# Performance work log

Hardware: AMD Instinct MI355X
Metric: run time of the kernel (lower is better)

## Reference

```python
import jax, jax.numpy as jnp
import numpy as np
from jax import lax

B, N, NIN, NOUT, K = 8, 4096, 64, 128, 32
RATIO, R = 0.25, 0.15
M = int(N * RATIO)
DIM = NIN + 4       # x_j concat 4 point-pair features


def setup_inputs() -> dict:
    key = jax.random.key(0)
    ks = jax.random.split(key, 10)
    x = jax.random.normal(ks[0], (B, N, NIN), jnp.float32)
    pos = jax.random.uniform(ks[1], (B, N, 3), jnp.float32)
    nrm = jax.random.normal(ks[2], (B, N, 3), jnp.float32)
    norm = nrm / jnp.linalg.norm(nrm, axis=-1, keepdims=True)
    batch = jnp.broadcast_to(jnp.arange(B, dtype=jnp.int32)[:, None], (B, N))
    s = 0.05
    W1 = jax.random.normal(ks[3], (DIM, DIM), jnp.float32) * s
    b1 = jnp.zeros((DIM,), jnp.float32)
    W2 = jax.random.normal(ks[4], (DIM, DIM), jnp.float32) * s
    b2 = jnp.zeros((DIM,), jnp.float32)
    W3 = jax.random.normal(ks[5], (DIM, NOUT), jnp.float32) * s
    b3 = jnp.zeros((NOUT,), jnp.float32)
    return dict(x=x, pos=pos, norm=norm, batch=batch,
                W1=W1, b1=b1, W2=W2, b2=b2, W3=W3, b3=b3)


def fps(pos):
    """Farthest point sampling, deterministic start at index 0. pos: [N,3] -> [M] int32."""
    n = pos.shape[0]
    def step(carry, _):
        dists, last = carry
        d = jnp.sum((pos - pos[last]) ** 2, axis=-1)
        dists = jnp.minimum(dists, d)
        nxt = jnp.argmax(dists).astype(jnp.int32)
        return (dists, nxt), last
    init = (jnp.full((n,), jnp.inf, pos.dtype), jnp.int32(0))
    (_, _), idx = lax.scan(step, init, None, length=M)
    return idx


def _angle(v1, v2):
    c = jnp.cross(v1, v2)
    return jnp.arctan2(jnp.linalg.norm(c, axis=-1), jnp.sum(v1 * v2, axis=-1))


def reference(x, pos, norm, batch, W1, b1, W2, b2, W3, b3):
    # batch is implicit in the leading B dim (equal-size clouds); arg kept for parity.
    idx = jax.vmap(fps)(pos)                                   # [B,M]
    pos_s = jnp.take_along_axis(pos, idx[..., None], axis=1)   # [B,M,3]
    norm_s = jnp.take_along_axis(norm, idx[..., None], axis=1) # [B,M,3]

    # radius neighbor search: K nearest within R per sampled center
    d2 = jnp.sum((pos_s[:, :, None, :] - pos[:, None, :, :]) ** 2, axis=-1)  # [B,M,N]
    masked = jnp.where(d2 <= R * R, d2, jnp.inf)
    negv, nbr = lax.top_k(-masked, K)                          # [B,M,K]
    valid = jnp.isfinite(negv)                                 # self always valid (d2=0)

    gather = jax.vmap(lambda a, i: a[i])                       # per-batch fancy gather
    x_j = gather(x, nbr)        # [B,M,K,NIN]
    pos_j = gather(pos, nbr)    # [B,M,K,3]
    norm_j = gather(norm, nbr)  # [B,M,K,3]

    d = pos_j - pos_s[:, :, None, :]                           # pos_j - pos_i
    n_i = jnp.broadcast_to(norm_s[:, :, None, :], norm_j.shape)
    ppf = jnp.stack([
        jnp.linalg.norm(d, axis=-1),
        _angle(n_i, d),
        _angle(norm_j, d),
        _angle(n_i, norm_j),
    ], axis=-1)                                                # [B,M,K,4]

    msg = jnp.concatenate([x_j, ppf], axis=-1)                 # [B,M,K,DIM]
    h = jax.nn.relu(msg @ W1 + b1)
    h = jax.nn.relu(h @ W2 + b2)
    h = jnp.where(valid[..., None], h, -jnp.inf)
    agg = jnp.max(h, axis=2)                                   # max aggregation [B,M,DIM]
    out = jax.nn.relu(agg @ W3 + b3)                           # global_nn [B,M,NOUT]
    return out, pos_s, idx
```

## Files before the change

kernel.cpp:

```cpp
#include <hip/hip_runtime.h>
#include <hip/hip_bf16.h>
#include <math.h>

#define BB 8
#define NN 4096
#define NIN 64
#define NOUTF 128
#define KNB 32
#define MM 1024
#define DIM 68
#define CAP 320

typedef float f32x2 __attribute__((ext_vector_type(2)));

__device__ __forceinline__ f32x2 pk_add(f32x2 a, f32x2 b)
{
    f32x2 d;
    asm("v_pk_add_f32 %0, %1, %2" : "=v"(d) : "v"(a), "v"(b));
    return d;
}
__device__ __forceinline__ f32x2 pk_mul(f32x2 a, f32x2 b)
{
    f32x2 d;
    asm("v_pk_mul_f32 %0, %1, %2" : "=v"(d) : "v"(a), "v"(b));
    return d;
}

__device__ __forceinline__ f32x2 pkmax(f32x2 a, f32x2 b)
{
    f32x2 r; r.x = fmaxf(a.x, b.x); r.y = fmaxf(a.y, b.y); return r;
}

template <int CTRL>
__device__ __forceinline__ float dppmax(float v)
{
    int m = __builtin_amdgcn_update_dpp(__float_as_int(v), __float_as_int(v),
                                        CTRL, 0xF, 0xF, false);
    return fmaxf(v, __int_as_float(m));
}

__global__ __launch_bounds__(256) void fps_kernel(
    const float* __restrict__ pos,
    int* __restrict__ idx_ws,
    float* __restrict__ out_pos_s, float* __restrict__ out_idx)
{
#pragma clang fp contract(off)
    __shared__ float4 posL[NN];
    __shared__ f32x2  slot[2][4];

    const int b    = blockIdx.x;
    const int tid  = threadIdx.x;
    const int wv   = tid >> 6;
    const int lane = tid & 63;
    const float* pb = pos + (size_t)b * NN * 3;

    f32x2 X[8], Y[8], Z[8], D[8];
#pragma unroll
    for (int j = 0; j < 8; ++j) {
        int pA = tid * 16 + 2 * j;
        X[j].x = pb[pA * 3 + 0]; X[j].y = pb[pA * 3 + 3];
        Y[j].x = pb[pA * 3 + 1]; Y[j].y = pb[pA * 3 + 4];
        Z[j].x = pb[pA * 3 + 2]; Z[j].y = pb[pA * 3 + 5];
        D[j].x = INFINITY;       D[j].y = INFINITY;
    }
#pragma unroll
    for (int j = 0; j < 16; ++j) {
        int p2 = tid + 256 * j;
        posL[p2] = make_float4(pb[p2 * 3 + 0], pb[p2 * 3 + 1],
                               pb[p2 * 3 + 2], 0.0f);
    }
    __syncthreads();

    int   last = 0;
    float lx = pb[0], ly = pb[1], lz = pb[2];

#pragma unroll 2
    for (int t = 0; t < MM; ++t) {
        if (tid == 0) {
            int base = b * MM + t;
            idx_ws[base]  = last;
            out_idx[base] = (float)last;
            out_pos_s[base * 3 + 0] = lx;
            out_pos_s[base * 3 + 1] = ly;
            out_pos_s[base * 3 + 2] = lz;
        }

        float nx = -lx, ny = -ly, nz = -lz;
        f32x2 nx2; nx2.x = nx; nx2.y = nx;
        f32x2 ny2; ny2.x = ny; ny2.y = ny;
        f32x2 nz2; nz2.x = nz; nz2.y = nz;

#pragma unroll
        for (int j = 0; j < 8; ++j) {
            f32x2 dx = pk_add(X[j], nx2);
            f32x2 dy = pk_add(Y[j], ny2);
            f32x2 dz = pk_add(Z[j], nz2);
            f32x2 xx = pk_mul(dx, dx);
            f32x2 yy = pk_mul(dy, dy);
            f32x2 zz = pk_mul(dz, dz);
            f32x2 s  = pk_add(pk_add(xx, yy), zz);
            D[j].x = fminf(D[j].x, s.x);
            D[j].y = fminf(D[j].y, s.y);
        }
        f32x2 m0 = pkmax(pkmax(D[0], D[1]), pkmax(D[2], D[3]));
        f32x2 m1 = pkmax(pkmax(D[4], D[5]), pkmax(D[6], D[7]));
        f32x2 mm = pkmax(m0, m1);
        float bv = fmaxf(mm.x, mm.y);

        int k0 = (D[0].x == bv) ? 0  : ((D[0].y == bv) ? 1  : 16);
        int k1 = (D[1].x == bv) ? 2  : ((D[1].y == bv) ? 3  : 16);
        int k2 = (D[2].x == bv) ? 4  : ((D[2].y == bv) ? 5  : 16);
        int k3 = (D[3].x == bv) ? 6  : ((D[3].y == bv) ? 7  : 16);
        int k4 = (D[4].x == bv) ? 8  : ((D[4].y == bv) ? 9  : 16);
        int k5 = (D[5].x == bv) ? 10 : ((D[5].y == bv) ? 11 : 16);
        int k6 = (D[6].x == bv) ? 12 : ((D[6].y == bv) ? 13 : 16);
        int k7 = (D[7].x == bv) ? 14 : ((D[7].y == bv) ? 15 : 16);
        k0 = min(k0, k4); k1 = min(k1, k5); k2 = min(k2, k6); k3 = min(k3, k7);
        k0 = min(k0, k2); k1 = min(k1, k3);
        int kmin = min(k0, k1);
        int p_cand = tid * 16 + kmin;

        float r = bv;
        r = dppmax<0x111>(r);
        r = dppmax<0x112>(r);
        r = dppmax<0x114>(r);
        r = dppmax<0x118>(r);
        r = dppmax<0x142>(r);
        r = dppmax<0x143>(r);
        float wmax = __int_as_float(__builtin_amdgcn_readlane(__float_as_int(r), 63));

        unsigned long long msk = __ballot(bv == wmax);
        int wl = __ffsll((long long)msk) - 1;
        int pwin_wave = __builtin_amdgcn_readlane(p_cand, wl);

        const int p_ = t & 1;
        if (lane == 0) {
            f32x2 sv; sv.x = wmax; sv.y = __int_as_float(pwin_wave);
            slot[p_][wv] = sv;
        }
        __syncthreads();

        f32x2 s0 = slot[p_][0], s1 = slot[p_][1];
        f32x2 s2 = slot[p_][2], s3 = slot[p_][3];
        float cv = s0.x; int ci = __float_as_int(s0.y);
        {
            int i1 = __float_as_int(s1.y);
            bool bt = (s1.x > cv) || (s1.x == cv && i1 < ci);
            cv = bt ? s1.x : cv; ci = bt ? i1 : ci;
        }
        {
            int i2 = __float_as_int(s2.y);
            bool bt = (s2.x > cv) || (s2.x == cv && i2 < ci);
            cv = bt ? s2.x : cv; ci = bt ? i2 : ci;
        }
        {
            int i3 = __float_as_int(s3.y);
            bool bt = (s3.x > cv) || (s3.x == cv && i3 < ci);
            cv = bt ? s3.x : cv; ci = bt ? i3 : ci;
        }

        float4 cw = posL[ci];
        last = ci; lx = cw.x; ly = cw.y; lz = cw.z;
    }
}

__global__ __launch_bounds__(256) void radius_kernel(
    const float* __restrict__ pos,
    const float* __restrict__ pos_s,
    int* __restrict__ nbr_ws, int* __restrict__ nvalid_ws)
{
    __shared__ float d2L[4][CAP];
    __shared__ int   idL[4][CAP];
    __shared__ int   cntL[4];

    const int wv = threadIdx.x >> 6, lane = threadIdx.x & 63;
    const int c = blockIdx.x * 4 + wv;
    const int b = c >> 10;
    const float RSQ = 0.0225f;

    if (lane == 0) cntL[wv] = 0;

    float cx = pos_s[c * 3 + 0];
    float cy = pos_s[c * 3 + 1];
    float cz = pos_s[c * 3 + 2];
    const float* pb = pos + (size_t)b * NN * 3;

    for (int it = 0; it < NN / 64; ++it) {
        int p = it * 64 + lane;
        float dx = __fsub_rn(cx, pb[p * 3 + 0]);
        float dy = __fsub_rn(cy, pb[p * 3 + 1]);
        float dz = __fsub_rn(cz, pb[p * 3 + 2]);
        float d2 = __fadd_rn(__fadd_rn(__fmul_rn(dx, dx), __fmul_rn(dy, dy)),
                             __fmul_rn(dz, dz));
        if (d2 <= RSQ) {
            int slot = atomicAdd(&cntL[wv], 1);
            if (slot < CAP) { d2L[wv][slot] = d2; idL[wv][slot] = p; }
        }
    }
    int n = cntL[wv];
    if (n > CAP) n = CAP;

    if (n <= KNB) {
        if (lane == 0) nvalid_ws[c] = n;
        if (lane < n) nbr_ws[c * KNB + lane] = idL[wv][lane];
    } else {
        if (lane == 0) nvalid_ws[c] = KNB;
        for (int a = lane; a < n; a += 64) {
            float da = d2L[wv][a]; int ia = idL[wv][a];
            int r = 0;
            for (int jj = 0; jj < n; ++jj) {
                float dj = d2L[wv][jj]; int ij = idL[wv][jj];
                r += (dj < da || (dj == da && ij < ia)) ? 1 : 0;
            }
            if (r < KNB) nbr_ws[c * KNB + r] = ia;
        }
    }
}

__device__ __forceinline__ float angle3(float ax, float ay, float az,
                                        float bx, float by, float bz)
{
    float cx = ay * bz - az * by;
    float cy = az * bx - ax * bz;
    float cz = ax * by - ay * bx;
    float cn = sqrtf(cx * cx + cy * cy + cz * cz);
    float dt = ax * bx + ay * by + az * bz;
    return atan2f(cn, dt);
}

__device__ __forceinline__ void layer_pass(const float* __restrict__ inL,
                                           const float* __restrict__ Ws,
                                           const float* __restrict__ bs,
                                           float* __restrict__ outL, int t)
{
    const int e = t & 63, wvi = t >> 6;
    for (int jg = wvi; jg < 17; jg += 4) {
        float ax = bs[jg * 4 + 0];
        float ay = bs[jg * 4 + 1];
        float az = bs[jg * 4 + 2];
        float aw = bs[jg * 4 + 3];
#pragma unroll 4
        for (int i = 0; i < DIM; ++i) {
            float m = inL[e * 69 + i];
            const float4 w = *reinterpret_cast<const float4*>(Ws + i * DIM + jg * 4);
            ax = fmaf(m, w.x, ax);
            ay = fmaf(m, w.y, ay);
            az = fmaf(m, w.z, az);
            aw = fmaf(m, w.w, aw);
        }
        outL[e * 69 + jg * 4 + 0] = fmaxf(ax, 0.0f);
        outL[e * 69 + jg * 4 + 1] = fmaxf(ay, 0.0f);
        outL[e * 69 + jg * 4 + 2] = fmaxf(az, 0.0f);
        outL[e * 69 + jg * 4 + 3] = fmaxf(aw, 0.0f);
    }
}

__global__ __launch_bounds__(256) void mlp_kernel(
    const float* __restrict__ x, const float* __restrict__ pos,
    const float* __restrict__ norm,
    const float* __restrict__ W1, const float* __restrict__ b1,
    const float* __restrict__ W2, const float* __restrict__ b2,
    const float* __restrict__ W3, const float* __restrict__ b3,
    const int* __restrict__ idx_ws, const float* __restrict__ pos_s,
    const int* __restrict__ nbr_ws, const int* __restrict__ nvalid_ws,
    float* __restrict__ out)
{
    __shared__ alignas(16) float W1s[DIM * DIM];
    __shared__ alignas(16) float W2s[DIM * DIM];
    __shared__ float b1s[DIM], b2s[DIM];
    __shared__ float msgL[64 * 69];
    __shared__ float h1L[64 * 69];
    __shared__ float aggL[2 * DIM];
    __shared__ int   nvL[2], jLs[64];

    const int t = threadIdx.x;
    const int cg0 = blockIdx.x * 2;

    for (int u = t; u < DIM * DIM; u += 256) { W1s[u] = W1[u]; W2s[u] = W2[u]; }
    if (t < DIM) { b1s[t] = b1[t]; b2s[t] = b2[t]; }
    if (t < 2) nvL[t] = min(nvalid_ws[cg0 + t], KNB);
    __syncthreads();

    const int e = t & 63, fc = t >> 6;
    const int lc = e >> 5, slot = e & 31;
    const int c = cg0 + lc;
    const int b = c >> 10;

    if (fc == 0) {
        int nv = nvL[lc];
        jLs[e] = (slot < nv) ? nbr_ws[c * KNB + slot] : 0;
    }
    __syncthreads();

    const int j = jLs[e];
    {
        const float* xj = x + ((size_t)b * NN + j) * NIN + fc * 16;
#pragma unroll
        for (int r = 0; r < 4; ++r) {
            float4 v = *reinterpret_cast<const float4*>(xj + r * 4);
            msgL[e * 69 + fc * 16 + r * 4 + 0] = v.x;
            msgL[e * 69 + fc * 16 + r * 4 + 1] = v.y;
            msgL[e * 69 + fc * 16 + r * 4 + 2] = v.z;
            msgL[e * 69 + fc * 16 + r * 4 + 3] = v.w;
        }
    }
    if (fc == 0) {
        float pix = pos_s[c * 3 + 0];
        float piy = pos_s[c * 3 + 1];
        float piz = pos_s[c * 3 + 2];
        int ic = idx_ws[c];
        const float* pj_ = pos  + ((size_t)b * NN + j) * 3;
        const float* nj_ = norm + ((size_t)b * NN + j) * 3;
        const float* ni_ = norm + ((size_t)b * NN + ic) * 3;
        float dx = pj_[0] - pix, dy = pj_[1] - piy, dz = pj_[2] - piz;
        float nix = ni_[0], niy = ni_[1], niz = ni_[2];
        float njx = nj_[0], njy = nj_[1], njz = nj_[2];
        msgL[e * 69 + 64] = sqrtf(dx * dx + dy * dy + dz * dz);
        msgL[e * 69 + 65] = angle3(nix, niy, niz, dx, dy, dz);
        msgL[e * 69 + 66] = angle3(njx, njy, njz, dx, dy, dz);
        msgL[e * 69 + 67] = angle3(nix, niy, niz, njx, njy, njz);
    }
    __syncthreads();

    layer_pass(msgL, W1s, b1s, h1L, t);
    __syncthreads();
    layer_pass(h1L, W2s, b2s, msgL, t);
    __syncthreads();

    if (t < 2 * DIM) {
        int cc = t / DIM, jf = t % DIM;
        int nv = nvL[cc];
        float v = -INFINITY;
        for (int s = 0; s < nv; ++s)
            v = fmaxf(v, msgL[(cc * 32 + s) * 69 + jf]);
        aggL[cc * DIM + jf] = v;
    }
    __syncthreads();

    {
        int cc = t >> 7, o = t & 127;
        int cgl = cg0 + cc;
        float acc = b3[o];
#pragma unroll 4
        for (int i = 0; i < DIM; ++i)
            acc = fmaf(aggL[cc * DIM + i], W3[i * NOUTF + o], acc);
        out[(size_t)cgl * NOUTF + o] = fmaxf(acc, 0.0f);
    }
}

extern "C" void kernel_launch(void* const* d_in, const int* in_sizes, int n_in,
                              void* d_out, int out_size, void* d_ws, size_t ws_size,
                              hipStream_t stream)
{
    const float* x    = (const float*)d_in[0];
    const float* pos  = (const float*)d_in[1];
    const float* norm = (const float*)d_in[2];
    const float* W1 = (const float*)d_in[4];
    const float* b1 = (const float*)d_in[5];
    const float* W2 = (const float*)d_in[6];
    const float* b2 = (const float*)d_in[7];
    const float* W3 = (const float*)d_in[8];
    const float* b3 = (const float*)d_in[9];

    float* out       = (float*)d_out;
    float* out_pos_s = out + (size_t)BB * MM * NOUTF;
    float* out_idx   = out_pos_s + (size_t)BB * MM * 3;

    char* ws = (char*)d_ws;
    int*   idx_ws    = (int*)ws;
    int*   nbr_ws    = (int*)(ws + 131072);
    int*   nvalid_ws = (int*)(ws + 131072 + (size_t)BB * MM * KNB * 4);

    fps_kernel<<<dim3(BB), dim3(256), 0, stream>>>(pos, idx_ws,
                                                   out_pos_s, out_idx);
    radius_kernel<<<dim3((BB * MM) / 4), dim3(256), 0, stream>>>(pos, out_pos_s,
                                                                 nbr_ws, nvalid_ws);
    mlp_kernel<<<dim3((BB * MM) / 2), dim3(256), 0, stream>>>(
        x, pos, norm, W1, b1, W2, b2, W3, b3,
        idx_ws, out_pos_s, nbr_ws, nvalid_ws, out);
}
```

Before: 1.013 ms.

## Carry winner coordinates in FPS reduction, buffer outputs, and register-block MLP layers

The FPS kernel no longer stages all positions in LDS. Each lane now picks its candidate's coordinates out of registers with a select tree and sends them through the per-wave slot, which removes the dependent LDS lookup after every iteration's barrier. Per-iteration global writes by thread 0 are replaced by LDS buffering, with one coalesced flush after the loop. The distance math is also fused into a single inline-asm block. Separately, the MLP layer pass now keeps four or five float4 accumulators per thread in a single loop over inputs, so each input value is read once instead of once per output group, at the cost of higher register pressure and a divergent fifth group in wave 0.

```diff
diff --git a/kernel.cpp b/kernel.cpp
--- a/kernel.cpp
+++ b/kernel.cpp
@@ -13,17 +13,21 @@
 
 typedef float f32x2 __attribute__((ext_vector_type(2)));
 
-__device__ __forceinline__ f32x2 pk_add(f32x2 a, f32x2 b)
-{
-    f32x2 d;
-    asm("v_pk_add_f32 %0, %1, %2" : "=v"(d) : "v"(a), "v"(b));
-    return d;
-}
-__device__ __forceinline__ f32x2 pk_mul(f32x2 a, f32x2 b)
-{
-    f32x2 d;
-    asm("v_pk_mul_f32 %0, %1, %2" : "=v"(d) : "v"(a), "v"(b));
-    return d;
+__device__ __forceinline__ f32x2 dist2pk(f32x2 X, f32x2 Y, f32x2 Z,
+                                         f32x2 nx, f32x2 ny, f32x2 nz)
+{
+    f32x2 dx, dy, dz;
+    asm("v_pk_add_f32 %0, %3, %6\n\t"
+        "v_pk_add_f32 %1, %4, %7\n\t"
+        "v_pk_add_f32 %2, %5, %8\n\t"
+        "v_pk_mul_f32 %0, %0, %0\n\t"
+        "v_pk_mul_f32 %1, %1, %1\n\t"
+        "v_pk_mul_f32 %2, %2, %2\n\t"
+        "v_pk_add_f32 %0, %0, %1\n\t"
+        "v_pk_add_f32 %0, %0, %2"
+        : "=&v"(dx), "=&v"(dy), "=&v"(dz)
+        : "v"(X), "v"(Y), "v"(Z), "v"(nx), "v"(ny), "v"(nz));
+    return dx;
 }
 
 __device__ __forceinline__ f32x2 pkmax(f32x2 a, f32x2 b)
@@ -45,8 +49,10 @@
     float* __restrict__ out_pos_s, float* __restrict__ out_idx)
 {
 #pragma clang fp contract(off)
-    __shared__ float4 posL[NN];
-    __shared__ f32x2  slot[2][4];
+    __shared__ float4 slotP[2][4];
+    __shared__ int    slotI[2][4];
+    __shared__ float4 emitP[MM];
+    __shared__ int    emitI[MM];
 
     const int b    = blockIdx.x;
     const int tid  = threadIdx.x;
@@ -63,13 +69,6 @@
         Z[j].x = pb[pA * 3 + 2]; Z[j].y = pb[pA * 3 + 5];
         D[j].x = INFINITY;       D[j].y = INFINITY;
     }
-#pragma unroll
-    for (int j = 0; j < 16; ++j) {
-        int p2 = tid + 256 * j;
-        posL[p2] = make_float4(pb[p2 * 3 + 0], pb[p2 * 3 + 1],
-                               pb[p2 * 3 + 2], 0.0f);
-    }
-    __syncthreads();
 
     int   last = 0;
     float lx = pb[0], ly = pb[1], lz = pb[2];
@@ -77,12 +76,8 @@
 #pragma unroll 2
     for (int t = 0; t < MM; ++t) {
         if (tid == 0) {
-            int base = b * MM + t;
-            idx_ws[base]  = last;
-            out_idx[base] = (float)last;
-            out_pos_s[base * 3 + 0] = lx;
-            out_pos_s[base * 3 + 1] = ly;
-            out_pos_s[base * 3 + 2] = lz;
+            emitP[t] = make_float4(lx, ly, lz, 0.0f);
+            emitI[t] = last;
         }
 
         float nx = -lx, ny = -ly, nz = -lz;
@@ -92,13 +87,7 @@
 
 #pragma unroll
         for (int j = 0; j < 8; ++j) {
-            f32x2 dx = pk_add(X[j], nx2);
-            f32x2 dy = pk_add(Y[j], ny2);
-            f32x2 dz = pk_add(Z[j], nz2);
-            f32x2 xx = pk_mul(dx, dx);
-            f32x2 yy = pk_mul(dy, dy);
-            f32x2 zz = pk_mul(dz, dz);
-            f32x2 s  = pk_add(pk_add(xx, yy), zz);
+            f32x2 s = dist2pk(X[j], Y[j], Z[j], nx2, ny2, nz2);
             D[j].x = fminf(D[j].x, s.x);
             D[j].y = fminf(D[j].y, s.y);
         }
@@ -120,6 +109,34 @@
         int kmin = min(k0, k1);
         int p_cand = tid * 16 + kmin;
 
+        int jj = kmin >> 1;
+        f32x2 xa = (jj & 1) ? X[1] : X[0];
+        f32x2 xb = (jj & 1) ? X[3] : X[2];
+        f32x2 xc = (jj & 1) ? X[5] : X[4];
+        f32x2 xd = (jj & 1) ? X[7] : X[6];
+        f32x2 xe = (jj & 2) ? xb : xa;
+        f32x2 xf = (jj & 2) ? xd : xc;
+        f32x2 xg = (jj & 4) ? xf : xe;
+        float bx = (kmin & 1) ? xg.y : xg.x;
+
+        f32x2 ya = (jj & 1) ? Y[1] : Y[0];
+        f32x2 yb = (jj & 1) ? Y[3] : Y[2];
+        f32x2 yc = (jj & 1) ? Y[5] : Y[4];
+        f32x2 yd = (jj & 1) ? Y[7] : Y[6];
+        f32x2 ye = (jj & 2) ? yb : ya;
+        f32x2 yf = (jj & 2) ? yd : yc;
+        f32x2 yg = (jj & 4) ? yf : ye;
+        float by = (kmin & 1) ? yg.y : yg.x;
+
+        f32x2 za = (jj & 1) ? Z[1] : Z[0];
+        f32x2 zb = (jj & 1) ? Z[3] : Z[2];
+        f32x2 zc = (jj & 1) ? Z[5] : Z[4];
+        f32x2 zd = (jj & 1) ? Z[7] : Z[6];
+        f32x2 ze = (jj & 2) ? zb : za;
+        f32x2 zf = (jj & 2) ? zd : zc;
+        f32x2 zg = (jj & 4) ? zf : ze;
+        float bz = (kmin & 1) ? zg.y : zg.x;
+
         float r = bv;
         r = dppmax<0x111>(r);
         r = dppmax<0x112>(r);
@@ -131,36 +148,49 @@
 
         unsigned long long msk = __ballot(bv == wmax);
         int wl = __ffsll((long long)msk) - 1;
-        int pwin_wave = __builtin_amdgcn_readlane(p_cand, wl);
 
         const int p_ = t & 1;
-        if (lane == 0) {
-            f32x2 sv; sv.x = wmax; sv.y = __int_as_float(pwin_wave);
-            slot[p_][wv] = sv;
+        if (lane == wl) {
+            slotP[p_][wv] = make_float4(bx, by, bz, bv);
+            slotI[p_][wv] = p_cand;
         }
         __syncthreads();
 
-        f32x2 s0 = slot[p_][0], s1 = slot[p_][1];
-        f32x2 s2 = slot[p_][2], s3 = slot[p_][3];
-        float cv = s0.x; int ci = __float_as_int(s0.y);
+        float4 e0 = slotP[p_][0], e1 = slotP[p_][1];
+        float4 e2 = slotP[p_][2], e3 = slotP[p_][3];
+        int    i0 = slotI[p_][0], i1 = slotI[p_][1];
+        int    i2 = slotI[p_][2], i3 = slotI[p_][3];
+
+        float cv = e0.w; int ci = i0;
+        float cx = e0.x, cy = e0.y, cz = e0.z;
         {
-            int i1 = __float_as_int(s1.y);
-            bool bt = (s1.x > cv) || (s1.x == cv && i1 < ci);
-            cv = bt ? s1.x : cv; ci = bt ? i1 : ci;
+            bool bt = (e1.w > cv) || (e1.w == cv && i1 < ci);
+            cv = bt ? e1.w : cv; ci = bt ? i1 : ci;
+            cx = bt ? e1.x : cx; cy = bt ? e1.y : cy; cz = bt ? e1.z : cz;
         }
         {
-            int i2 = __float_as_int(s2.y);
-            bool bt = (s2.x > cv) || (s2.x == cv && i2 < ci);
-            cv = bt ? s2.x : cv; ci = bt ? i2 : ci;
+            bool bt = (e2.w > cv) || (e2.w == cv && i2 < ci);
+            cv = bt ? e2.w : cv; ci = bt ? i2 : ci;
+            cx = bt ? e2.x : cx; cy = bt ? e2.y : cy; cz = bt ? e2.z : cz;
         }
         {
-            int i3 = __float_as_int(s3.y);
-            bool bt = (s3.x > cv) || (s3.x == cv && i3 < ci);
-            cv = bt ? s3.x : cv; ci = bt ? i3 : ci;
-        }
-
-        float4 cw = posL[ci];
-        last = ci; lx = cw.x; ly = cw.y; lz = cw.z;
+            bool bt = (e3.w > cv) || (e3.w == cv && i3 < ci);
+            cv = bt ? e3.w : cv; ci = bt ? i3 : ci;
+            cx = bt ? e3.x : cx; cy = bt ? e3.y : cy; cz = bt ? e3.z : cz;
+        }
+        last = ci; lx = cx; ly = cy; lz = cz;
+    }
+
+    __syncthreads();
+    for (int u = tid; u < MM; u += 256) {
+        float4 rec = emitP[u];
+        int    id  = emitI[u];
+        int base = b * MM + u;
+        idx_ws[base]  = id;
+        out_idx[base] = (float)id;
+        out_pos_s[base * 3 + 0] = rec.x;
+        out_pos_s[base * 3 + 1] = rec.y;
+        out_pos_s[base * 3 + 2] = rec.z;
     }
 }
 
@@ -228,30 +258,56 @@
     return atan2f(cn, dt);
 }
 
+__device__ __forceinline__ float4 fma4(float m, float4 w, float4 a)
+{
+    a.x = fmaf(m, w.x, a.x);
+    a.y = fmaf(m, w.y, a.y);
+    a.z = fmaf(m, w.z, a.z);
+    a.w = fmaf(m, w.w, a.w);
+    return a;
+}
+
 __device__ __forceinline__ void layer_pass(const float* __restrict__ inL,
                                            const float* __restrict__ Ws,
                                            const float* __restrict__ bs,
                                            float* __restrict__ outL, int t)
 {
     const int e = t & 63, wvi = t >> 6;
-    for (int jg = wvi; jg < 17; jg += 4) {
-        float ax = bs[jg * 4 + 0];
-        float ay = bs[jg * 4 + 1];
-        float az = bs[jg * 4 + 2];
-        float aw = bs[jg * 4 + 3];
+    const bool has5 = (wvi == 0);
+    const int j0 = wvi * 4, j1 = (wvi + 4) * 4, j2 = (wvi + 8) * 4,
+              j3 = (wvi + 12) * 4, j4 = 64;
+
+    float4 a0 = *reinterpret_cast<const float4*>(bs + j0);
+    float4 a1 = *reinterpret_cast<const float4*>(bs + j1);
+    float4 a2 = *reinterpret_cast<const float4*>(bs + j2);
+    float4 a3 = *reinterpret_cast<const float4*>(bs + j3);
+    float4 a4 = has5 ? *reinterpret_cast<const float4*>(bs + j4)
+                     : make_float4(0.f, 0.f, 0.f, 0.f);
+
+    const float* row = inL + e * 69;
 #pragma unroll 4
-        for (int i = 0; i < DIM; ++i) {
-            float m = inL[e * 69 + i];
-            const float4 w = *reinterpret_cast<const float4*>(Ws + i * DIM + jg * 4);
-            ax = fmaf(m, w.x, ax);
-            ay = fmaf(m, w.y, ay);
-            az = fmaf(m, w.z, az);
-            aw = fmaf(m, w.w, aw);
-        }
-        outL[e * 69 + jg * 4 + 0] = fmaxf(ax, 0.0f);
-        outL[e * 69 + jg * 4 + 1] = fmaxf(ay, 0.0f);
-        outL[e * 69 + jg * 4 + 2] = fmaxf(az, 0.0f);
-        outL[e * 69 + jg * 4 + 3] = fmaxf(aw, 0.0f);
+    for (int i = 0; i < DIM; ++i) {
+        float m = row[i];
+        const float* wr = Ws + i * DIM;
+        a0 = fma4(m, *reinterpret_cast<const float4*>(wr + j0), a0);
+        a1 = fma4(m, *reinterpret_cast<const float4*>(wr + j1), a1);
+        a2 = fma4(m, *reinterpret_cast<const float4*>(wr + j2), a2);
+        a3 = fma4(m, *reinterpret_cast<const float4*>(wr + j3), a3);
+        if (has5) a4 = fma4(m, *reinterpret_cast<const float4*>(wr + j4), a4);
+    }
+
+    float* orow = outL + e * 69;
+    orow[j0 + 0] = fmaxf(a0.x, 0.f); orow[j0 + 1] = fmaxf(a0.y, 0.f);
+    orow[j0 + 2] = fmaxf(a0.z, 0.f); orow[j0 + 3] = fmaxf(a0.w, 0.f);
+    orow[j1 + 0] = fmaxf(a1.x, 0.f); orow[j1 + 1] = fmaxf(a1.y, 0.f);
+    orow[j1 + 2] = fmaxf(a1.z, 0.f); orow[j1 + 3] = fmaxf(a1.w, 0.f);
+    orow[j2 + 0] = fmaxf(a2.x, 0.f); orow[j2 + 1] = fmaxf(a2.y, 0.f);
+    orow[j2 + 2] = fmaxf(a2.z, 0.f); orow[j2 + 3] = fmaxf(a2.w, 0.f);
+    orow[j3 + 0] = fmaxf(a3.x, 0.f); orow[j3 + 1] = fmaxf(a3.y, 0.f);
+    orow[j3 + 2] = fmaxf(a3.z, 0.f); orow[j3 + 3] = fmaxf(a3.w, 0.f);
+    if (has5) {
+        orow[64] = fmaxf(a4.x, 0.f); orow[65] = fmaxf(a4.y, 0.f);
+        orow[66] = fmaxf(a4.z, 0.f); orow[67] = fmaxf(a4.w, 0.f);
     }
 }
 
@@ -267,7 +323,8 @@
 {
     __shared__ alignas(16) float W1s[DIM * DIM];
     __shared__ alignas(16) float W2s[DIM * DIM];
-    __shared__ float b1s[DIM], b2s[DIM];
+    __shared__ alignas(16) float b1s[DIM];
+    __shared__ alignas(16) float b2s[DIM];
     __shared__ float msgL[64 * 69];
     __shared__ float h1L[64 * 69];
     __shared__ float aggL[2 * DIM];
```

Result: slower. 1.497 ms (+47.9%).
